# Performance work log

Hardware: AMD Instinct MI355X
Metric: run time of the kernel (lower is better)

The kernel has to match this reference:

```python
import jax, jax.numpy as jnp
import numpy as np
import math

B, T, D, H = 4, 2048, 1024, 16
ND = D // H  # head dim = 64


def setup_inputs() -> dict:
    key = jax.random.key(0)
    ks = jax.random.split(key, 12)
    s = 1.0 / math.sqrt(D)
    inp = {
        "q": jax.random.normal(ks[0], (B, T, D), jnp.float32),
        "k": jax.random.normal(ks[1], (B, T, D), jnp.float32),
        "v": jax.random.normal(ks[2], (B, T, D), jnp.float32),
        # nn.Linear params: weight [out,in], bias [out]
        "wq": jax.random.normal(ks[3], (D, D), jnp.float32) * s,
        "bq": jax.random.normal(ks[4], (D,), jnp.float32) * s,
        "wk": jax.random.normal(ks[5], (D, D), jnp.float32) * s,
        "bk": jax.random.normal(ks[6], (D,), jnp.float32) * s,
        "wv": jax.random.normal(ks[7], (D, D), jnp.float32) * s,
        "bv": jax.random.normal(ks[8], (D,), jnp.float32) * s,
        "wo": jax.random.normal(ks[9], (D, D), jnp.float32) * s,
        "bo": jax.random.normal(ks[10], (D,), jnp.float32) * s,
        # causal mask: 1 where attending allowed, 0 -> -inf
        "mask": jnp.tril(jnp.ones((T, T), jnp.int32)),
    }
    return inp


def reference(q, k, v, wq, bq, wk, bk, wv, bv, wo, bo, mask):
    batch, time, dim = q.shape
    n_d = dim // H
    # NOTE: original module (faithfully reproduced bug) computes k and v from q
    Q = q @ wq.T + bq
    K = q @ wk.T + bk
    V = q @ wv.T + bv
    # [B, T, D] -> [B, H, T, nd]
    Q = Q.reshape(batch, time, H, n_d).transpose(0, 2, 1, 3)
    K = K.reshape(batch, time, H, n_d).transpose(0, 2, 1, 3)
    V = V.reshape(batch, time, H, n_d).transpose(0, 2, 1, 3)
    score = jnp.einsum("bhqd,bhkd->bhqk", Q, K) / math.sqrt(n_d)
    score = jnp.where(mask == 0, -jnp.inf, score)
    # original uses nn.Softmax(dim=-2): normalize over the QUERY axis
    attn = jax.nn.softmax(score, axis=-2)
    out = jnp.einsum("bhqk,bhkd->bhqd", attn, V)
    out = out.transpose(0, 2, 1, 3).reshape(batch, time, dim)
    return out @ wo.T + bo
```

## Files before the change

### kernel.cpp

```cpp
#include <hip/hip_runtime.h>
#include <stdint.h>

#define B_  4
#define T_  2048
#define D_  1024
#define H_  16
#define ND_ 64
#define M_  (B_ * T_)

typedef unsigned short u16;
typedef __bf16 bf8  __attribute__((ext_vector_type(8)));
typedef float  f4   __attribute__((ext_vector_type(4)));
typedef u16    u16x8 __attribute__((ext_vector_type(8)));

__device__ inline float bf2f(u16 b) {
    unsigned int x = ((unsigned int)b) << 16;
    return __builtin_bit_cast(float, x);
}
__device__ inline u16 f2bf(float f) {
    unsigned int x = __builtin_bit_cast(unsigned int, f);
    x += 0x7fffu + ((x >> 16) & 1u);
    return (u16)(x >> 16);
}
__device__ inline f4 mfma16(bf8 a, bf8 b, f4 c) {
    return __builtin_amdgcn_mfma_f32_16x16x32_bf16(a, b, c, 0, 0, 0);
}
__device__ inline void async16(const void* g, void* l) {
    auto gp = reinterpret_cast<const __attribute__((address_space(1))) unsigned int*>(
        reinterpret_cast<uintptr_t>(g));
    auto lp = reinterpret_cast<__attribute__((address_space(3))) unsigned int*>(
        reinterpret_cast<uintptr_t>(l));
    __builtin_amdgcn_global_load_lds(gp, lp, 16, 0, 0);
}

__global__ __launch_bounds__(256)
void cvt_bf16(const float* __restrict__ in, u16* __restrict__ out, int n) {
    int i = (blockIdx.x * blockDim.x + threadIdx.x) * 8;
    if (i + 8 <= n) {
        float4 a = *(const float4*)(in + i);
        float4 b = *(const float4*)(in + i + 4);
        u16x8 o;
        o[0] = f2bf(a.x); o[1] = f2bf(a.y); o[2] = f2bf(a.z); o[3] = f2bf(a.w);
        o[4] = f2bf(b.x); o[5] = f2bf(b.y); o[6] = f2bf(b.z); o[7] = f2bf(b.w);
        *(u16x8*)(out + i) = o;
    }
}

template <int MODE>
__global__ __launch_bounds__(256, 2)
void gemm_bt(const u16* __restrict__ A, const u16* __restrict__ W,
             const float* __restrict__ bias, void* __restrict__ CoutV) {
    constexpr int K = 1024;
    constexpr int N = 1024;
    __shared__ __attribute__((aligned(16))) u16 sA[128 * 32];
    __shared__ __attribute__((aligned(16))) u16 sB[128 * 32];
    const int tid  = threadIdx.x;
    const int wave = tid >> 6;
    const int lane = tid & 63;
    const int m0 = blockIdx.y * 128;
    const int n0 = blockIdx.x * 128;
    const int wm = (wave & 1) * 64;
    const int wn = (wave >> 1) * 64;

    f4 acc[4][4] = {};

    const int srow = wave * 32 + (lane >> 2);
    const int scol = (lane & 3) * 8;
    const u16* gA = A + (size_t)(m0 + srow) * K + scol;
    const u16* gB = W + (size_t)(n0 + srow) * K + scol;
    u16* lA0 = sA + (wave * 32) * 32;
    u16* lA1 = sA + (wave * 32 + 16) * 32;
    u16* lB0 = sB + (wave * 32) * 32;
    u16* lB1 = sB + (wave * 32 + 16) * 32;

    const int row = lane & 15;
    const int qo  = (lane >> 4) * 8;

    for (int k0 = 0; k0 < K; k0 += 32) {
        async16(gA + k0, lA0);
        async16(gA + k0 + (size_t)16 * K, lA1);
        async16(gB + k0, lB0);
        async16(gB + k0 + (size_t)16 * K, lB1);
        __syncthreads();

        bf8 af[4], bfr[4];
#pragma unroll
        for (int i = 0; i < 4; i++)
            af[i] = *(const bf8*)(sA + (wm + i * 16 + row) * 32 + qo);
#pragma unroll
        for (int i = 0; i < 4; i++)
            bfr[i] = *(const bf8*)(sB + (wn + i * 16 + row) * 32 + qo);
#pragma unroll
        for (int mi = 0; mi < 4; mi++)
#pragma unroll
            for (int ni = 0; ni < 4; ni++)
                acc[mi][ni] = mfma16(af[mi], bfr[ni], acc[mi][ni]);
        __syncthreads();
    }

#pragma unroll
    for (int ni = 0; ni < 4; ni++) {
        const int n = n0 + wn + ni * 16 + row;
        const float bv = bias[n];
#pragma unroll
        for (int mi = 0; mi < 4; mi++) {
#pragma unroll
            for (int r = 0; r < 4; r++) {
                const int m = m0 + wm + mi * 16 + (lane >> 4) * 4 + r;
                const float v = acc[mi][ni][r] + bv;
                if (MODE == 1) {
                    size_t idx = (((size_t)((m >> 11) * H_ + (n >> 6)) * T_) + (m & (T_ - 1))) * ND_ +
                                 (n & (ND_ - 1));
                    ((u16*)CoutV)[idx] = f2bf(v);
                } else if (MODE == 2) {
                    size_t idx = ((size_t)(((m >> 11) * H_ + (n >> 6)) * ND_ + (n & (ND_ - 1)))) * T_ +
                                 (m & (T_ - 1));
                    ((u16*)CoutV)[idx] = f2bf(v);
                } else {
                    ((float*)CoutV)[(size_t)m * N + n] = v;
                }
            }
        }
    }
}

__global__ __launch_bounds__(256)
void col_sum(const u16* __restrict__ Qh, const u16* __restrict__ Kh,
             float* __restrict__ Ic) {
    const int bh   = blockIdx.y;
    const int wave = threadIdx.x >> 6;
    const int lane = threadIdx.x & 63;
    const int l15  = lane & 15;
    const int quad = lane >> 4;
    const int qo   = quad * 8;
    const u16* Qb = Qh + (size_t)bh * T_ * ND_;
    const u16* Kb = Kh + (size_t)bh * T_ * ND_;

#pragma unroll
    for (int half = 0; half < 2; half++) {
        const int kb   = half ? (31 - (int)blockIdx.x) : (int)blockIdx.x;
        const int k0   = kb * 64 + wave * 16;
        const int kcol = k0 + l15;
        const bf8 b0 = *(const bf8*)(Kb + (size_t)kcol * ND_ + qo);
        const bf8 b1 = *(const bf8*)(Kb + (size_t)kcol * ND_ + 32 + qo);

        f4 acc = {0.f, 0.f, 0.f, 0.f};
        {
            const u16* q0 = Qb + (size_t)(k0 + l15) * ND_;
            bf8 a0 = *(const bf8*)(q0 + qo);
            bf8 a1 = *(const bf8*)(q0 + 32 + qo);
            f4 s = {0.f, 0.f, 0.f, 0.f};
            s = mfma16(a0, b0, s);
            s = mfma16(a1, b1, s);
#pragma unroll
            for (int r = 0; r < 4; r++)
                acc[r] += (quad * 4 + r >= l15) ? __expf(s[r] * 0.125f) : 0.f;
        }
        int qt = k0 + 16;
        for (; qt + 32 <= T_; qt += 32) {
            const u16* q0 = Qb + (size_t)(qt + l15) * ND_;
            const u16* q1 = Qb + (size_t)(qt + 16 + l15) * ND_;
            bf8 a00 = *(const bf8*)(q0 + qo);
            bf8 a01 = *(const bf8*)(q0 + 32 + qo);
            bf8 a10 = *(const bf8*)(q1 + qo);
            bf8 a11 = *(const bf8*)(q1 + 32 + qo);
            f4 s0 = {0.f, 0.f, 0.f, 0.f}, s1 = {0.f, 0.f, 0.f, 0.f};
            s0 = mfma16(a00, b0, s0);
            s0 = mfma16(a01, b1, s0);
            s1 = mfma16(a10, b0, s1);
            s1 = mfma16(a11, b1, s1);
#pragma unroll
            for (int r = 0; r < 4; r++) acc[r] += __expf(s0[r] * 0.125f);
#pragma unroll
            for (int r = 0; r < 4; r++) acc[r] += __expf(s1[r] * 0.125f);
        }
        if (qt < T_) {
            const u16* q0 = Qb + (size_t)(qt + l15) * ND_;
            bf8 a00 = *(const bf8*)(q0 + qo);
            bf8 a01 = *(const bf8*)(q0 + 32 + qo);
            f4 s0 = {0.f, 0.f, 0.f, 0.f};
            s0 = mfma16(a00, b0, s0);
            s0 = mfma16(a01, b1, s0);
#pragma unroll
            for (int r = 0; r < 4; r++) acc[r] += __expf(s0[r] * 0.125f);
        }
        float l = acc[0] + acc[1] + acc[2] + acc[3];
        l += __shfl_xor(l, 16);
        l += __shfl_xor(l, 32);
        if (lane < 16) Ic[(size_t)bh * T_ + kcol] = 1.f / l;
    }
}

__global__ __launch_bounds__(256, 4)
void attn_out(const u16* __restrict__ Qh, const u16* __restrict__ Kh,
              const u16* __restrict__ Vt, const float* __restrict__ Ic,
              u16* __restrict__ AO) {
    __shared__ __attribute__((aligned(16))) u16 sK[64 * 72];
    __shared__ __attribute__((aligned(16))) u16 sVt[64 * 72];
    __shared__ __attribute__((aligned(16))) u16 sP[4][32 * 72];
    const int bh   = blockIdx.x;
    const int b    = bh >> 4;
    const int h    = bh & 15;
    const int qb   = (int)(gridDim.y - 1 - blockIdx.y) * 128;
    const int tid  = threadIdx.x;
    const int wave = tid >> 6;
    const int lane = tid & 63;
    const int l15  = lane & 15;
    const int quad = lane >> 4;
    const int qo   = quad * 8;

    const u16* Qb = Qh + (size_t)bh * T_ * ND_;
    const u16* Kb = Kh + (size_t)bh * T_ * ND_;
    const u16* Vb = Vt + (size_t)bh * ND_ * T_;
    const float* ic = Ic + (size_t)bh * T_;

    const int qw = qb + wave * 32;
    bf8 aq[2][2];
#pragma unroll
    for (int qs = 0; qs < 2; qs++)
#pragma unroll
        for (int dh = 0; dh < 2; dh++)
            aq[qs][dh] = *(const bf8*)(Qb + (size_t)(qw + qs * 16 + l15) * ND_ + dh * 32 + qo);

    f4 o[2][4] = {};

    const int sr = tid >> 3;
    const int sc = (tid & 7) * 8;
    const int kend = qb + 128;

    u16x8 pk0 = *(const u16x8*)(Kb + (size_t)sr * ND_ + sc);
    u16x8 pk1 = *(const u16x8*)(Kb + (size_t)(sr + 32) * ND_ + sc);
    u16x8 pv0 = *(const u16x8*)(Vb + (size_t)sr * T_ + sc);
    u16x8 pv1 = *(const u16x8*)(Vb + (size_t)(sr + 32) * T_ + sc);

    for (int kt = 0; kt < kend; kt += 64) {
        *(u16x8*)(sK + sr * 72 + sc) = pk0;
        *(u16x8*)(sK + (sr + 32) * 72 + sc) = pk1;
        *(u16x8*)(sVt + sr * 72 + sc) = pv0;
        *(u16x8*)(sVt + (sr + 32) * 72 + sc) = pv1;
        __syncthreads();

        const int ktn = kt + 64;
        if (ktn < kend) {
            pk0 = *(const u16x8*)(Kb + (size_t)(ktn + sr) * ND_ + sc);
            pk1 = *(const u16x8*)(Kb + (size_t)(ktn + sr + 32) * ND_ + sc);
            pv0 = *(const u16x8*)(Vb + (size_t)sr * T_ + ktn + sc);
            pv1 = *(const u16x8*)(Vb + (size_t)(sr + 32) * T_ + ktn + sc);
        }

#pragma unroll
        for (int ks = 0; ks < 4; ks++) {
            bf8 kb0 = *(const bf8*)(sK + (ks * 16 + l15) * 72 + qo);
            bf8 kb1 = *(const bf8*)(sK + (ks * 16 + l15) * 72 + 32 + qo);
            const int kg = kt + ks * 16 + l15;
            const float il = ic[kg];
#pragma unroll
            for (int qs = 0; qs < 2; qs++) {
                f4 s = {0.f, 0.f, 0.f, 0.f};
                s = mfma16(aq[qs][0], kb0, s);
                s = mfma16(aq[qs][1], kb1, s);
#pragma unroll
                for (int r = 0; r < 4; r++) {
                    const int qg = qw + qs * 16 + quad * 4 + r;
                    const float p = (kg <= qg) ? __expf(s[r] * 0.125f) * il : 0.f;
                    sP[wave][(qs * 16 + quad * 4 + r) * 72 + ks * 16 + l15] = f2bf(p);
                }
            }
        }
#pragma unroll
        for (int st = 0; st < 2; st++) {
            bf8 ap0 = *(const bf8*)(&sP[wave][(l15) * 72 + st * 32 + qo]);
            bf8 ap1 = *(const bf8*)(&sP[wave][(16 + l15) * 72 + st * 32 + qo]);
#pragma unroll
            for (int ds = 0; ds < 4; ds++) {
                bf8 bv = *(const bf8*)(sVt + (ds * 16 + l15) * 72 + st * 32 + qo);
                o[0][ds] = mfma16(ap0, bv, o[0][ds]);
                o[1][ds] = mfma16(ap1, bv, o[1][ds]);
            }
        }
        __syncthreads();
    }

#pragma unroll
    for (int qs = 0; qs < 2; qs++)
#pragma unroll
        for (int ds = 0; ds < 4; ds++)
#pragma unroll
            for (int r = 0; r < 4; r++) {
                const int q = qw + qs * 16 + quad * 4 + r;
                const int d = ds * 16 + l15;
                AO[((size_t)(b * T_ + q)) * D_ + h * ND_ + d] = f2bf(o[qs][ds][r]);
            }
}

extern "C" void kernel_launch(void* const* d_in, const int* in_sizes, int n_in,
                              void* d_out, int out_size, void* d_ws, size_t ws_size,
                              hipStream_t stream) {
    (void)in_sizes; (void)n_in; (void)out_size; (void)ws_size;
    const float* q  = (const float*)d_in[0];
    const float* wq = (const float*)d_in[3];
    const float* bq = (const float*)d_in[4];
    const float* wk = (const float*)d_in[5];
    const float* bk = (const float*)d_in[6];
    const float* wv = (const float*)d_in[7];
    const float* bv = (const float*)d_in[8];
    const float* wo = (const float*)d_in[9];
    const float* bo = (const float*)d_in[10];

    const size_t SZ = (size_t)M_ * D_;
    const size_t WSZ = (size_t)D_ * D_;
    u16* Qh  = (u16*)d_ws;
    u16* Kh  = Qh + SZ;
    u16* Vtr = Kh + SZ;
    u16* qbf = Vtr + SZ;
    u16* AO  = qbf;
    u16* wqb = qbf + SZ;
    u16* wkb = wqb + WSZ;
    u16* wvb = wkb + WSZ;
    u16* wob = wvb + WSZ;
    float* Ic = (float*)(wob + WSZ);

    cvt_bf16<<<dim3(SZ / 8 / 256), 256, 0, stream>>>(q, qbf, (int)SZ);
    cvt_bf16<<<dim3(WSZ / 8 / 256), 256, 0, stream>>>(wq, wqb, (int)WSZ);
    cvt_bf16<<<dim3(WSZ / 8 / 256), 256, 0, stream>>>(wk, wkb, (int)WSZ);
    cvt_bf16<<<dim3(WSZ / 8 / 256), 256, 0, stream>>>(wv, wvb, (int)WSZ);
    cvt_bf16<<<dim3(WSZ / 8 / 256), 256, 0, stream>>>(wo, wob, (int)WSZ);

    dim3 gp(D_ / 128, M_ / 128);
    gemm_bt<1><<<gp, 256, 0, stream>>>(qbf, wqb, bq, Qh);
    gemm_bt<1><<<gp, 256, 0, stream>>>(qbf, wkb, bk, Kh);
    gemm_bt<2><<<gp, 256, 0, stream>>>(qbf, wvb, bv, Vtr);

    dim3 gs(16, B_ * H_);
    col_sum<<<gs, 256, 0, stream>>>(Qh, Kh, Ic);

    dim3 ga(B_ * H_, T_ / 128);
    attn_out<<<ga, 256, 0, stream>>>(Qh, Kh, Vtr, Ic, AO);

    gemm_bt<0><<<gp, 256, 0, stream>>>(AO, wob, bo, d_out);
}
```

Before: 466.1 us.

## Stage Q tiles in shared memory for column-sum and widen per-block key strips

The col_sum kernel now handles 128-key strips per block, with each wave covering 32 keys. Q rows are double-buffered through LDS with a register prefetch, so one Q tile is shared by all four waves instead of each wave reading Q from global memory on its own. The grid is halved to keep the same balanced strip pairing. The trade-off is a __syncthreads per 32-row tile, fewer blocks in the grid, and masking checks across the first 128 rows.

```diff
diff --git a/kernel.cpp b/kernel.cpp
--- a/kernel.cpp
+++ b/kernel.cpp
@@ -127,67 +127,73 @@
 __global__ __launch_bounds__(256)
 void col_sum(const u16* __restrict__ Qh, const u16* __restrict__ Kh,
              float* __restrict__ Ic) {
+    __shared__ __attribute__((aligned(16))) u16 sQ[2][32 * 72];
     const int bh   = blockIdx.y;
-    const int wave = threadIdx.x >> 6;
-    const int lane = threadIdx.x & 63;
+    const int tid  = threadIdx.x;
+    const int wave = tid >> 6;
+    const int lane = tid & 63;
     const int l15  = lane & 15;
     const int quad = lane >> 4;
     const int qo   = quad * 8;
+    const int sr   = tid >> 3;
+    const int sc   = (tid & 7) * 8;
     const u16* Qb = Qh + (size_t)bh * T_ * ND_;
     const u16* Kb = Kh + (size_t)bh * T_ * ND_;
 
 #pragma unroll
     for (int half = 0; half < 2; half++) {
-        const int kb   = half ? (31 - (int)blockIdx.x) : (int)blockIdx.x;
-        const int k0   = kb * 64 + wave * 16;
-        const int kcol = k0 + l15;
-        const bf8 b0 = *(const bf8*)(Kb + (size_t)kcol * ND_ + qo);
-        const bf8 b1 = *(const bf8*)(Kb + (size_t)kcol * ND_ + 32 + qo);
-
-        f4 acc = {0.f, 0.f, 0.f, 0.f};
-        {
-            const u16* q0 = Qb + (size_t)(k0 + l15) * ND_;
-            bf8 a0 = *(const bf8*)(q0 + qo);
-            bf8 a1 = *(const bf8*)(q0 + 32 + qo);
-            f4 s = {0.f, 0.f, 0.f, 0.f};
-            s = mfma16(a0, b0, s);
-            s = mfma16(a1, b1, s);
-#pragma unroll
-            for (int r = 0; r < 4; r++)
-                acc[r] += (quad * 4 + r >= l15) ? __expf(s[r] * 0.125f) : 0.f;
-        }
-        int qt = k0 + 16;
-        for (; qt + 32 <= T_; qt += 32) {
-            const u16* q0 = Qb + (size_t)(qt + l15) * ND_;
-            const u16* q1 = Qb + (size_t)(qt + 16 + l15) * ND_;
-            bf8 a00 = *(const bf8*)(q0 + qo);
-            bf8 a01 = *(const bf8*)(q0 + 32 + qo);
-            bf8 a10 = *(const bf8*)(q1 + qo);
-            bf8 a11 = *(const bf8*)(q1 + 32 + qo);
-            f4 s0 = {0.f, 0.f, 0.f, 0.f}, s1 = {0.f, 0.f, 0.f, 0.f};
-            s0 = mfma16(a00, b0, s0);
-            s0 = mfma16(a01, b1, s0);
-            s1 = mfma16(a10, b0, s1);
-            s1 = mfma16(a11, b1, s1);
-#pragma unroll
-            for (int r = 0; r < 4; r++) acc[r] += __expf(s0[r] * 0.125f);
-#pragma unroll
-            for (int r = 0; r < 4; r++) acc[r] += __expf(s1[r] * 0.125f);
-        }
-        if (qt < T_) {
-            const u16* q0 = Qb + (size_t)(qt + l15) * ND_;
-            bf8 a00 = *(const bf8*)(q0 + qo);
-            bf8 a01 = *(const bf8*)(q0 + 32 + qo);
-            f4 s0 = {0.f, 0.f, 0.f, 0.f};
-            s0 = mfma16(a00, b0, s0);
-            s0 = mfma16(a01, b1, s0);
-#pragma unroll
-            for (int r = 0; r < 4; r++) acc[r] += __expf(s0[r] * 0.125f);
-        }
-        float l = acc[0] + acc[1] + acc[2] + acc[3];
-        l += __shfl_xor(l, 16);
-        l += __shfl_xor(l, 32);
-        if (lane < 16) Ic[(size_t)bh * T_ + kcol] = 1.f / l;
+        const int strip = half ? (15 - (int)blockIdx.x) : (int)blockIdx.x;
+        const int c0  = strip * 128;
+        const int c0w = c0 + wave * 32;
+        bf8 b0[2], b1[2];
+#pragma unroll
+        for (int g = 0; g < 2; g++) {
+            b0[g] = *(const bf8*)(Kb + (size_t)(c0w + g * 16 + l15) * ND_ + qo);
+            b1[g] = *(const bf8*)(Kb + (size_t)(c0w + g * 16 + l15) * ND_ + 32 + qo);
+        }
+        float acc[2][4] = {};
+        int p = 0;
+        u16x8 pq = *(const u16x8*)(Qb + (size_t)(c0 + sr) * ND_ + sc);
+        for (int qt = c0; qt < T_; qt += 32) {
+            *(u16x8*)(&sQ[p][sr * 72 + sc]) = pq;
+            __syncthreads();
+            if (qt + 32 < T_)
+                pq = *(const u16x8*)(Qb + (size_t)(qt + 32 + sr) * ND_ + sc);
+            const bool masked = qt < c0 + 128;
+#pragma unroll
+            for (int sub = 0; sub < 2; sub++) {
+                const int rho = sub * 16 + l15;
+                bf8 a0 = *(const bf8*)(&sQ[p][rho * 72 + qo]);
+                bf8 a1 = *(const bf8*)(&sQ[p][rho * 72 + 32 + qo]);
+#pragma unroll
+                for (int g = 0; g < 2; g++) {
+                    f4 s = {0.f, 0.f, 0.f, 0.f};
+                    s = mfma16(a0, b0[g], s);
+                    s = mfma16(a1, b1[g], s);
+                    if (masked) {
+#pragma unroll
+                        for (int r = 0; r < 4; r++) {
+                            const int qg = qt + sub * 16 + quad * 4 + r;
+                            const int cg = c0w + g * 16 + l15;
+                            acc[g][r] += (qg >= cg) ? __expf(s[r] * 0.125f) : 0.f;
+                        }
+                    } else {
+#pragma unroll
+                        for (int r = 0; r < 4; r++)
+                            acc[g][r] += __expf(s[r] * 0.125f);
+                    }
+                }
+            }
+            p ^= 1;
+        }
+        __syncthreads();
+#pragma unroll
+        for (int g = 0; g < 2; g++) {
+            float l = acc[g][0] + acc[g][1] + acc[g][2] + acc[g][3];
+            l += __shfl_xor(l, 16);
+            l += __shfl_xor(l, 32);
+            if (lane < 16) Ic[(size_t)bh * T_ + c0w + g * 16 + l15] = 1.f / l;
+        }
     }
 }
 
@@ -331,8 +337,8 @@
     gemm_bt<1><<<gp, 256, 0, stream>>>(qbf, wkb, bk, Kh);
     gemm_bt<2><<<gp, 256, 0, stream>>>(qbf, wvb, bv, Vtr);
 
-    dim3 gs(16, B_ * H_);
-    col_sum<<<gs, 256, 0, stream>>>(Qh, Kh, Ic);
+    dim3 gcs(8, B_ * H_);
+    col_sum<<<gcs, 256, 0, stream>>>(Qh, Kh, Ic);
 
     dim3 ga(B_ * H_, T_ / 128);
     attn_out<<<ga, 256, 0, stream>>>(Qh, Kh, Vtr, Ic, AO);
```

Measured after the change: 395.9 us. 15.1% less time.
